# Performance work log

Measured on AMD Instinct MI355X. Metric: run time of the kernel, lower is better.

Reference implementation:

```python
import jax, jax.numpy as jnp
import numpy as np

B, S, E, H = 2, 2048, 1024, 16
D = E // H  # head_dim = 64


def setup_inputs() -> dict:
    key = jax.random.key(0)
    ks = jax.random.split(key, 9)
    w = 0.02
    return {
        "values": jax.random.normal(ks[0], (B, S, E), dtype=jnp.float32),
        "keys": jax.random.normal(ks[1], (B, S, E), dtype=jnp.float32),
        "queries": jax.random.normal(ks[2], (B, S, E), dtype=jnp.float32),
        "Wv": jax.random.normal(ks[3], (E, E), dtype=jnp.float32) * w,
        "bv": jnp.zeros((E,), dtype=jnp.float32),
        "Wk": jax.random.normal(ks[4], (E, E), dtype=jnp.float32) * w,
        "bk": jnp.zeros((E,), dtype=jnp.float32),
        "Wq": jax.random.normal(ks[5], (E, E), dtype=jnp.float32) * w,
        "bq": jnp.zeros((E,), dtype=jnp.float32),
    }


def reference(values, keys, queries, Wv, bv, Wk, bk, Wq, bq):
    b = queries.shape[0]
    v_len, k_len, q_len = values.shape[1], keys.shape[1], queries.shape[1]
    # torch.nn.Linear: y = x @ W^T + b
    k = (keys @ Wk.T + bk).reshape(b, k_len, H, D)
    v = (values @ Wv.T + bv).reshape(b, v_len, H, D)
    q = (queries @ Wq.T + bq).reshape(b, q_len, H, D)
    # NOTE: faithful to source, scaling is by sqrt(q_len), not sqrt(head_dim)
    energy = jnp.einsum('bqhd,bkhd->bhqk', q, k) / jnp.sqrt(jnp.float32(q_len))
    attn = jax.nn.softmax(energy, axis=3)
    # NOTE: faithful to source einsum 'bhqk,bvhd->bqhd' (k and v summed separately)
    out = jnp.einsum('bhqk,bvhd->bqhd', attn, v)
    return out
```

## Files before the change

### kernel.cpp

```cpp
#include <hip/hip_runtime.h>


#define BB 2
#define SS 2048
#define EE 1024

constexpr int NSC = 128;
constexpr int SC  = SS / NSC;

__global__ void colsum_kernel(const float* __restrict__ values,
                              float* __restrict__ colsum) {
    const int tid = threadIdx.x;
    const int b   = blockIdx.x % BB;
    const int sc  = blockIdx.x / BB;
    const int e0  = tid * 4;
    const float* p =
        values + (size_t)b * SS * EE + (size_t)sc * SC * EE + e0;
    float a0 = 0.f, a1 = 0.f, a2 = 0.f, a3 = 0.f;
    #pragma unroll
    for (int s = 0; s < SC; ++s) {
        float4 u = *reinterpret_cast<const float4*>(p + (size_t)s * EE);
        a0 += u.x; a1 += u.y; a2 += u.z; a3 += u.w;
    }
    float* dst = colsum + b * EE + e0;
    atomicAdd(dst + 0, a0);
    atomicAdd(dst + 1, a1);
    atomicAdd(dst + 2, a2);
    atomicAdd(dst + 3, a3);
}

__global__ void matvec_kernel(const float* __restrict__ Wv,
                              const float* __restrict__ bv,
                              const float* __restrict__ colsum,
                              float* __restrict__ out_row) {
    const int gtid = blockIdx.x * blockDim.x + threadIdx.x;
    const int wave = gtid >> 6;
    const int lane = threadIdx.x & 63;
    const int b = wave / EE;
    const int j = wave % EE;
    const float* w = Wv + (size_t)j * EE;
    const float* x = colsum + b * EE;
    float acc = 0.f;
    #pragma unroll
    for (int i = 0; i < EE / 256; ++i) {
        int e = i * 256 + lane * 4;
        float4 wv = *reinterpret_cast<const float4*>(w + e);
        float4 xv = *reinterpret_cast<const float4*>(x + e);
        acc += wv.x * xv.x + wv.y * xv.y + wv.z * xv.z + wv.w * xv.w;
    }
    #pragma unroll
    for (int off = 32; off; off >>= 1) acc += __shfl_down(acc, off, 64);
    if (lane == 0)
        out_row[b * EE + j] = acc + (float)SS * bv[j];
}

__global__ void bcast_kernel(const float* __restrict__ out_row,
                             float* __restrict__ out) {
    const size_t idx = (size_t)blockIdx.x * blockDim.x + threadIdx.x;
    const size_t pos = idx * 4;
    const int e = (int)(pos & (EE - 1));
    const int b = (int)(pos / ((size_t)SS * EE));
    const float4 v = *reinterpret_cast<const float4*>(out_row + b * EE + e);
    *reinterpret_cast<float4*>(out + pos) = v;
}

extern "C" void kernel_launch(void* const* d_in, const int* in_sizes, int n_in,
                              void* d_out, int out_size, void* d_ws, size_t ws_size,
                              hipStream_t stream) {
    const float* values = (const float*)d_in[0];
    const float* Wv     = (const float*)d_in[3];
    const float* bv     = (const float*)d_in[4];
    float* out = (float*)d_out;

    float* colsum  = (float*)d_ws;
    float* out_row = colsum + BB * EE;

    hipMemsetAsync(colsum, 0, BB * EE * sizeof(float), stream);

    colsum_kernel<<<BB * NSC, 256, 0, stream>>>(values, colsum);

    matvec_kernel<<<(BB * EE) / 4, 256, 0, stream>>>(Wv, bv, colsum, out_row);

    const size_t total = (size_t)BB * SS * EE;
    bcast_kernel<<<(unsigned int)(total / 4 / 256), 256, 0, stream>>>(
        out_row, out);
}
```

Before: 121.1 us.

## Replace atomic colsum and memset with partial sums reduced inside matvec

The column-sum kernel now writes per-chunk partial sums to workspace instead of issuing atomicAdds, which removes the memset launch and atomic contention. A new fused kernel reduces the 128 partials into shared memory and then computes the matvec, each of its 32 blocks handling 64 output rows. This cuts one launch and the atomics, but the matvec now runs on only 32 blocks with each redundantly re-reducing 512KB of partials, which may underuse the GPU.

```diff
diff --git a/kernel.cpp b/kernel.cpp
--- a/kernel.cpp
+++ b/kernel.cpp
@@ -5,53 +5,65 @@
 #define SS 2048
 #define EE 1024
 
-constexpr int NSC = 128;
-constexpr int SC  = SS / NSC;
+constexpr int NCH = 128;
+constexpr int CH  = SS / NCH;
 
-__global__ void colsum_kernel(const float* __restrict__ values,
-                              float* __restrict__ colsum) {
+__global__ void colsum_partial_kernel(const float* __restrict__ values,
+                                      float* __restrict__ partial) {
     const int tid = threadIdx.x;
-    const int b   = blockIdx.x % BB;
-    const int sc  = blockIdx.x / BB;
+    const int b   = blockIdx.x & 1;
+    const int c   = blockIdx.x >> 1;
     const int e0  = tid * 4;
     const float* p =
-        values + (size_t)b * SS * EE + (size_t)sc * SC * EE + e0;
-    float a0 = 0.f, a1 = 0.f, a2 = 0.f, a3 = 0.f;
+        values + (size_t)b * SS * EE + (size_t)c * CH * EE + e0;
+    float4 a = {0.f, 0.f, 0.f, 0.f};
     #pragma unroll
-    for (int s = 0; s < SC; ++s) {
+    for (int s = 0; s < CH; ++s) {
         float4 u = *reinterpret_cast<const float4*>(p + (size_t)s * EE);
-        a0 += u.x; a1 += u.y; a2 += u.z; a3 += u.w;
+        a.x += u.x; a.y += u.y; a.z += u.z; a.w += u.w;
     }
-    float* dst = colsum + b * EE + e0;
-    atomicAdd(dst + 0, a0);
-    atomicAdd(dst + 1, a1);
-    atomicAdd(dst + 2, a2);
-    atomicAdd(dst + 3, a3);
+    *reinterpret_cast<float4*>(partial + ((size_t)(b * NCH + c)) * EE + e0) = a;
 }
 
-__global__ void matvec_kernel(const float* __restrict__ Wv,
-                              const float* __restrict__ bv,
-                              const float* __restrict__ colsum,
-                              float* __restrict__ out_row) {
-    const int gtid = blockIdx.x * blockDim.x + threadIdx.x;
-    const int wave = gtid >> 6;
-    const int lane = threadIdx.x & 63;
-    const int b = wave / EE;
-    const int j = wave % EE;
-    const float* w = Wv + (size_t)j * EE;
-    const float* x = colsum + b * EE;
-    float acc = 0.f;
+__global__ void reduce_matvec_kernel(const float* __restrict__ Wv,
+                                     const float* __restrict__ bv,
+                                     const float* __restrict__ partial,
+                                     float* __restrict__ out_row) {
+    __shared__ float sm[EE];
+    const int tid = threadIdx.x;
+    const int b   = blockIdx.x >> 4;
+    const int jg  = blockIdx.x & 15;
+    {
+        const int e0 = tid * 4;
+        const float* p = partial + (size_t)b * NCH * EE + e0;
+        float4 a = {0.f, 0.f, 0.f, 0.f};
+        #pragma unroll 8
+        for (int c = 0; c < NCH; ++c) {
+            float4 u = *reinterpret_cast<const float4*>(p + (size_t)c * EE);
+            a.x += u.x; a.y += u.y; a.z += u.z; a.w += u.w;
+        }
+        *reinterpret_cast<float4*>(sm + e0) = a;
+    }
+    __syncthreads();
+    const int wave = tid >> 6;
+    const int lane = tid & 63;
     #pragma unroll
-    for (int i = 0; i < EE / 256; ++i) {
-        int e = i * 256 + lane * 4;
-        float4 wv = *reinterpret_cast<const float4*>(w + e);
-        float4 xv = *reinterpret_cast<const float4*>(x + e);
-        acc += wv.x * xv.x + wv.y * xv.y + wv.z * xv.z + wv.w * xv.w;
+    for (int jj = 0; jj < 16; ++jj) {
+        const int j = jg * 64 + wave * 16 + jj;
+        const float* w = Wv + (size_t)j * EE;
+        float acc = 0.f;
+        #pragma unroll
+        for (int i = 0; i < EE / 256; ++i) {
+            int e = i * 256 + lane * 4;
+            float4 wv = *reinterpret_cast<const float4*>(w + e);
+            float4 xv = *reinterpret_cast<const float4*>(sm + e);
+            acc += wv.x * xv.x + wv.y * xv.y + wv.z * xv.z + wv.w * xv.w;
+        }
+        #pragma unroll
+        for (int off = 32; off; off >>= 1) acc += __shfl_down(acc, off, 64);
+        if (lane == 0)
+            out_row[b * EE + j] = acc + (float)SS * bv[j];
     }
-    #pragma unroll
-    for (int off = 32; off; off >>= 1) acc += __shfl_down(acc, off, 64);
-    if (lane == 0)
-        out_row[b * EE + j] = acc + (float)SS * bv[j];
 }
 
 __global__ void bcast_kernel(const float* __restrict__ out_row,
@@ -72,14 +84,12 @@
     const float* bv     = (const float*)d_in[4];
     float* out = (float*)d_out;
 
-    float* colsum  = (float*)d_ws;
-    float* out_row = colsum + BB * EE;
+    float* partial = (float*)d_ws;
+    float* out_row = partial + (size_t)BB * NCH * EE;
 
-    hipMemsetAsync(colsum, 0, BB * EE * sizeof(float), stream);
+    colsum_partial_kernel<<<BB * NCH, 256, 0, stream>>>(values, partial);
 
-    colsum_kernel<<<BB * NSC, 256, 0, stream>>>(values, colsum);
-
-    matvec_kernel<<<(BB * EE) / 4, 256, 0, stream>>>(Wv, bv, colsum, out_row);
+    reduce_matvec_kernel<<<32, 256, 0, stream>>>(Wv, bv, partial, out_row);
 
     const size_t total = (size_t)BB * SS * EE;
     bcast_kernel<<<(unsigned int)(total / 4 / 256), 256, 0, stream>>>(
```

Result: slower. 124.0 us (+2.4%).
